# Performance work log

Measured on AMD Instinct MI355X. Metric: run time of the kernel, lower is better.

Reference implementation:

```python
import jax, jax.numpy as jnp
import numpy as np
import math

EPS = 1e-8
LN_EPS = 1e-5
B, S, E, NH = 2, 2048, 1024, 4
DH = E // NH


def setup_inputs() -> dict:
    key = jax.random.key(0)
    ks = jax.random.split(key, 7)
    std_g = math.sqrt(2.0 / (5.0 * 3 * E))
    return {
        "q": jax.random.normal(ks[0], (B, S, E), dtype=jnp.float32),
        "k": jax.random.normal(ks[1], (B, S, E), dtype=jnp.float32),
        "v": jax.random.normal(ks[2], (B, S, E), dtype=jnp.float32),
        "igate_w": jax.random.normal(ks[3], (NH, 3 * E), dtype=jnp.float32) * std_g,
        "igate_b": jax.random.normal(ks[4], (NH,), dtype=jnp.float32) * 0.1,
        "fgate_w": jax.random.normal(ks[5], (NH, 3 * E), dtype=jnp.float32) * std_g,
        "fgate_b": jnp.linspace(3.4, 6.0, NH, dtype=jnp.float32),
        "out_w": jnp.zeros((E,), dtype=jnp.float32),  # residual affine weight (scale = 1 + out_w)
    }


def _mlstm_cell(q, k, v, igate_w, igate_b, fgate_w, fgate_b, out_w):
    Bq, Sq, Eq = q.shape
    # gate pre-activations from concatenated q,k,v: [B,S,NH]
    if_in = jnp.concatenate([q, k, v], axis=-1)
    ig = jnp.einsum("bsf,hf->bsh", if_in, igate_w) + igate_b
    fg = jnp.einsum("bsf,hf->bsh", if_in, fgate_w) + fgate_b
    ig = jnp.transpose(ig, (0, 2, 1))[..., None]  # [B,NH,S,1]
    fg = jnp.transpose(fg, (0, 2, 1))[..., None]  # [B,NH,S,1]

    # split heads: [B,NH,S,DH]
    qh = q.reshape(Bq, Sq, NH, DH).transpose(0, 2, 1, 3)
    kh = k.reshape(Bq, Sq, NH, DH).transpose(0, 2, 1, 3)
    vh = v.reshape(Bq, Sq, NH, DH).transpose(0, 2, 1, 3)

    # cumulative log forget gates -> causal decay matrix (log space)
    log_fg = jax.nn.log_sigmoid(fg)                           # [B,NH,S,1]
    cs = jnp.cumsum(log_fg, axis=2)                           # [B,NH,S,1]
    cs_shift = jnp.concatenate([jnp.zeros_like(cs[:, :, :1]), cs[:, :, :-1]], axis=2)
    # log_fg_matrix[i,j] = cumsum[i] - cumsum[j-1], masked causal
    logfg_mat = cs - jnp.swapaxes(cs_shift, -2, -1)           # [B,NH,S,S]
    ltr = jnp.tril(jnp.ones((Sq, Sq), dtype=bool))
    logfg_mat = jnp.where(ltr, logfg_mat, -jnp.inf)
    log_D = logfg_mat + jnp.swapaxes(ig, -2, -1)              # + igate row broadcast [B,NH,1,S]

    max_log_D = jnp.max(log_D, axis=-1, keepdims=True)        # [B,NH,S,1]
    D = jnp.exp(log_D - max_log_D)                            # stabilized decay matrix

    qk = jnp.einsum("bhsd,bhtd->bhst", qh, kh / math.sqrt(DH))
    C = qk * D
    sum_C_abs = jnp.abs(jnp.sum(C, axis=-1, keepdims=True))
    normaliser = jnp.maximum(sum_C_abs, jnp.exp(-max_log_D))  # robust normalizer
    C_norm = C / (normaliser + EPS)
    h = jnp.einsum("bhst,bhtd->bhsd", C_norm, vh)             # [B,NH,S,DH]

    # MultiHeadLayerNorm == group_norm with NH groups, per-channel residual weight
    mean = jnp.mean(h, axis=-1, keepdims=True)
    var = jnp.mean((h - mean) ** 2, axis=-1, keepdims=True)
    h_norm = (h - mean) / jnp.sqrt(var + LN_EPS)
    scale = (1.0 + out_w).reshape(1, NH, 1, DH)
    h_norm = h_norm * scale

    return h_norm.transpose(0, 2, 1, 3).reshape(Bq, Sq, Eq)


def reference(q, k, v, igate_w, igate_b, fgate_w, fgate_b, out_w):
    return _mlstm_cell(q, k, v, igate_w, igate_b, fgate_w, fgate_b, out_w)
```

## Files before the change

kernel.cpp:

```cpp
#include <hip/hip_runtime.h>
#include <hip/hip_bf16.h>
#include <math.h>

#define Bb  2
#define Ss  2048
#define Ee  1024
#define NHh 4
#define DHh 256
#define BH  (Bb*NHh)
#define TI  64
#define TIB 128
#define TJ  32
#define NT2 (Ss/TI)
#define NTB (Ss/TIB)
#define NJT (Ss/TJ)

typedef short        s8v   __attribute__((ext_vector_type(8)));
typedef float        f4v   __attribute__((ext_vector_type(4)));
typedef float        f16v  __attribute__((ext_vector_type(16)));
typedef unsigned int u4v   __attribute__((ext_vector_type(4)));
typedef unsigned int u2v   __attribute__((ext_vector_type(2)));

__device__ inline unsigned pkbf2(float a, float b) {
    __hip_bfloat162 h2 = __float22bfloat162_rn(float2{a, b});
    unsigned u;
    __builtin_memcpy(&u, &h2, 4);
    return u;
}

__device__ inline void async16(const void* g, void* l) {
    __builtin_amdgcn_global_load_lds(
        (const __attribute__((address_space(1))) void*)g,
        (__attribute__((address_space(3))) void*)l, 16, 0, 0);
}

__global__ __launch_bounds__(256) void gates_prep_kernel(
    const float* __restrict__ q, const float* __restrict__ k, const float* __restrict__ v,
    const float* __restrict__ igw, const float* __restrict__ igb,
    const float* __restrict__ fgw, const float* __restrict__ fgb,
    float* __restrict__ ig_out, float* __restrict__ fg_out,
    unsigned short* __restrict__ Kimg, unsigned short* __restrict__ Vimg)
{
    int bidx = blockIdx.x;
    int tid = threadIdx.x;

    if (bidx >= 512) {
        int pidx = bidx - 512;
        int bh = pidx >> 6, jt = pidx & 63;
        int b = bh >> 2, h = bh & 3;
        int J0 = jt * TJ;
        const size_t hoff = (size_t)h * DHh;
        unsigned short* Kt = Kimg + (size_t)pidx * 1024 * 8;
        unsigned short* Vt = Vimg + (size_t)pidx * 1024 * 8;

        {
            int kR = tid >> 3, kc0 = tid & 7;
            const float* src = k + ((size_t)(b * Ss + J0 + kR)) * Ee + hoff;
#pragma unroll
            for (int p = 0; p < 4; p++) {
                int cc = kc0 + 8 * p;
                float4 x0 = ((const float4*)(src + cc * 8))[0];
                float4 x1 = ((const float4*)(src + cc * 8))[1];
                u4v wv;
                wv.x = pkbf2(x0.x, x0.y); wv.y = pkbf2(x0.z, x0.w);
                wv.z = pkbf2(x1.x, x1.y); wv.w = pkbf2(x1.z, x1.w);
                *(u4v*)&Kt[(kR * 32 + (cc ^ (kR & 7))) * 8] = wv;
            }
        }
        {
            int vdp = tid & 127, vjb = tid >> 7;
            int d0 = vdp * 2;
#pragma unroll
            for (int p = 0; p < 2; p++) {
                int jc = vjb + 2 * p;
                const float* vbase = v + ((size_t)(b * Ss + J0 + jc * 8)) * Ee + hoff + d0;
                float2 e0 = *(const float2*)(vbase);
                float2 e1 = *(const float2*)(vbase + Ee);
                float2 e2 = *(const float2*)(vbase + 2 * Ee);
                float2 e3 = *(const float2*)(vbase + 3 * Ee);
                float2 e4 = *(const float2*)(vbase + 4 * Ee);
                float2 e5 = *(const float2*)(vbase + 5 * Ee);
                float2 e6 = *(const float2*)(vbase + 6 * Ee);
                float2 e7 = *(const float2*)(vbase + 7 * Ee);
                int swz = jc ^ (vdp & 3);
                u4v w0, w1;
                w0.x = pkbf2(e0.x, e1.x); w0.y = pkbf2(e2.x, e3.x);
                w0.z = pkbf2(e4.x, e5.x); w0.w = pkbf2(e6.x, e7.x);
                w1.x = pkbf2(e0.y, e1.y); w1.y = pkbf2(e2.y, e3.y);
                w1.z = pkbf2(e4.y, e5.y); w1.w = pkbf2(e6.y, e7.y);
                *(u4v*)&Vt[(d0 * 4 + swz) * 8] = w0;
                *(u4v*)&Vt[((d0 + 1) * 4 + swz) * 8] = w1;
            }
        }
        return;
    }

    int sc = bidx >> 1, hp = bidx & 1;
    __shared__ float wl[4][3072];
    __shared__ float pw[4][8];

#pragma unroll
    for (int c = 0; c < 4; c++) {
        int h = hp * 2 + (c >> 1);
        const float* src = ((c & 1) ? fgw : igw) + (size_t)h * 3 * Ee;
        for (int idx = tid * 4; idx < 3 * Ee; idx += 1024)
            *(float4*)&wl[c][idx] = *(const float4*)(src + idx);
    }
    __syncthreads();

    int c4 = tid * 4;
    int w = tid >> 6, lane = tid & 63;

    for (int sp = 0; sp < 8; sp++) {
        int bs0 = sc * 16 + sp * 2;
        float4 qa = *(const float4*)(q + (size_t)bs0 * Ee + c4);
        float4 ka = *(const float4*)(k + (size_t)bs0 * Ee + c4);
        float4 va = *(const float4*)(v + (size_t)bs0 * Ee + c4);
        float4 qb = *(const float4*)(q + (size_t)(bs0 + 1) * Ee + c4);
        float4 kb = *(const float4*)(k + (size_t)(bs0 + 1) * Ee + c4);
        float4 vb = *(const float4*)(v + (size_t)(bs0 + 1) * Ee + c4);
        float red[8];
#pragma unroll
        for (int c = 0; c < 4; c++) {
            const float* wc = wl[c];
            float4 wq = *(const float4*)&wc[c4];
            float4 wk = *(const float4*)&wc[Ee + c4];
            float4 wv = *(const float4*)&wc[2 * Ee + c4];
            float x0 = qa.x*wq.x + qa.y*wq.y + qa.z*wq.z + qa.w*wq.w
                     + ka.x*wk.x + ka.y*wk.y + ka.z*wk.z + ka.w*wk.w
                     + va.x*wv.x + va.y*wv.y + va.z*wv.z + va.w*wv.w;
            float x1 = qb.x*wq.x + qb.y*wq.y + qb.z*wq.z + qb.w*wq.w
                     + kb.x*wk.x + kb.y*wk.y + kb.z*wk.z + kb.w*wk.w
                     + vb.x*wv.x + vb.y*wv.y + vb.z*wv.z + vb.w*wv.w;
            for (int off = 32; off > 0; off >>= 1) {
                x0 += __shfl_down(x0, off, 64);
                x1 += __shfl_down(x1, off, 64);
            }
            red[c] = x0; red[4 + c] = x1;
        }
        __syncthreads();
        if (lane == 0) {
#pragma unroll
            for (int c = 0; c < 8; c++) pw[w][c] = red[c];
        }
        __syncthreads();
        if (tid < 8) {
            float t = pw[0][tid] + pw[1][tid] + pw[2][tid] + pw[3][tid];
            int rr = tid >> 2, cc = tid & 3;
            int h = hp * 2 + (cc >> 1);
            int bs = bs0 + rr;
            int b = bs >> 11, s = bs & 2047;
            size_t o = ((size_t)(b * NHh + h)) * Ss + s;
            if (cc & 1) fg_out[o] = t + fgb[h];
            else        ig_out[o] = t + igb[h];
        }
    }
}

#define CHUNK 8
__global__ __launch_bounds__(256) void scan_kernel(
    const float* __restrict__ ig, const float* __restrict__ fg,
    float* __restrict__ a_out, float* __restrict__ M_out, float* __restrict__ nf_out)
{
    int bh = blockIdx.x;
    int tid = threadIdx.x;
    const float* igp = ig + (size_t)bh * Ss;
    const float* fgp = fg + (size_t)bh * Ss;
    int s0 = tid * CHUNK;

    float ls[CHUNK], cs[CHUNK];
    float tot = 0.f;
#pragma unroll
    for (int c = 0; c < CHUNK; c++) {
        float x = fgp[s0 + c];
        float l = fminf(x, 0.f) - log1pf(expf(-fabsf(x)));
        ls[c] = l; tot += l; cs[c] = tot;
    }
    __shared__ float sc[256];
    sc[tid] = tot; __syncthreads();
    for (int off = 1; off < 256; off <<= 1) {
        float add = (tid >= off) ? sc[tid - off] : 0.f;
        __syncthreads();
        sc[tid] += add;
        __syncthreads();
    }
    float excl = sc[tid] - tot;

    float av[CHUNK], pmax[CHUNK];
    float tmax = -INFINITY;
#pragma unroll
    for (int c = 0; c < CHUNK; c++) {
        float csf  = excl + cs[c];
        float csm1 = csf - ls[c];
        float a = igp[s0 + c] - csm1;
        av[c] = a;
        tmax = fmaxf(tmax, a);
        pmax[c] = tmax;
        cs[c] = csf;
    }
    __shared__ float sm[256];
    sm[tid] = tmax; __syncthreads();
    for (int off = 1; off < 256; off <<= 1) {
        float other = (tid >= off) ? sm[tid - off] : -INFINITY;
        __syncthreads();
        sm[tid] = fmaxf(sm[tid], other);
        __syncthreads();
    }
    float emax = (tid > 0) ? sm[tid - 1] : -INFINITY;
#pragma unroll
    for (int c = 0; c < CHUNK; c++) {
        float M = fmaxf(emax, pmax[c]);
        size_t o = (size_t)bh * Ss + s0 + c;
        a_out[o]  = av[c];
        M_out[o]  = M;
        nf_out[o] = expf(-cs[c] - M);
    }
}

__global__ __launch_bounds__(256, 2) void mlstm_eq(
    const float* __restrict__ qp,
    const unsigned short* __restrict__ Kimg, const unsigned short* __restrict__ Vimg,
    const float* __restrict__ a_ws, const float* __restrict__ M_ws,
    float* __restrict__ outF, float* __restrict__ Hpart, float* __restrict__ rsbuf)
{
    int bidx = blockIdx.x;
    int bh = bidx & 7;
    int w  = bidx >> 3;
    int pr = w >> 3;
    int c8 = w & 7;
    int b = bh >> 2, h = bh & 3;
    int tid = threadIdx.x;

    const int nA = 4 * pr + 4;
    const int s0 = (c8 * 68) >> 3;
    const int e0 = ((c8 + 1) * 68) >> 3;
    int qA = 0;
#pragma unroll
    for (int cc = 0; cc < 8; cc++)
        if ((((cc + 1) * 68) >> 3) <= nA) qA++;

    const size_t hoff = (size_t)h * DHh;
    const size_t HP = (size_t)Bb * Ss * Ee;

    __shared__ unsigned short KF[2][1024 * 8];
    __shared__ unsigned short VF[2][1024 * 8];
    __shared__ unsigned short PF[512 * 8];
    __shared__ float a_s[2][TJ];
    __shared__ float rs_s[TIB];

    const int iq   = tid >> 6;
    const int lane = tid & 63;
    const int lm = lane & 15, q4 = lane >> 4;
    const float inv_sqrt_dh = 0.0625f;

    const unsigned short* Kb = Kimg + (size_t)(bh * NJT) * 1024 * 8;
    const unsigned short* Vb = Vimg + (size_t)(bh * NJT) * 1024 * 8;
    const float* a_base = a_ws + (size_t)bh * Ss;

    for (int pc = 0; pc < 2; pc++) {
        int T, jt_beg, jt_end, ord;
        if (pc == 0) {
            if (s0 >= nA) continue;
            T = pr; jt_beg = s0;
            jt_end = (e0 < nA) ? e0 : nA;
            ord = c8;
        } else {
            if (e0 <= nA) continue;
            T = 15 - pr;
            jt_beg = (s0 > nA ? s0 : nA) - nA;
            jt_end = e0 - nA;
            ord = c8 - qA;
        }
        const int I0 = T * TIB;
        float* Hdst = (ord == 0) ? outF : (Hpart + (size_t)(ord - 1) * HP);

        s8v qf0[8], qf1[8];
        {
            const float* qrow0 = qp + ((size_t)(b * Ss + I0 + iq * 16 + lm)) * Ee + hoff;
            const float* qrow1 = qrow0 + (size_t)64 * Ee;
#pragma unroll
            for (int ks = 0; ks < 8; ks++) {
                const float4* p0 = (const float4*)(qrow0 + ks * 32 + q4 * 8);
                float4 x0 = p0[0], x1 = p0[1];
                union { s8v v; unsigned u[4]; } rr;
                rr.u[0] = pkbf2(x0.x, x0.y);
                rr.u[1] = pkbf2(x0.z, x0.w);
                rr.u[2] = pkbf2(x1.x, x1.y);
                rr.u[3] = pkbf2(x1.z, x1.w);
                qf0[ks] = rr.v;
                const float4* p1 = (const float4*)(qrow1 + ks * 32 + q4 * 8);
                float4 y0 = p1[0], y1 = p1[1];
                union { s8v v; unsigned u[4]; } ss;
                ss.u[0] = pkbf2(y0.x, y0.y);
                ss.u[1] = pkbf2(y0.z, y0.w);
                ss.u[2] = pkbf2(y1.x, y1.y);
                ss.u[3] = pkbf2(y1.z, y1.w);
                qf1[ks] = ss.v;
            }
        }
        const int  i_row0 = I0 + iq * 16 + lm;
        const int  i_row1 = i_row0 + 64;
        const float Mi0 = M_ws[(size_t)bh * Ss + i_row0];
        const float Mi1 = M_ws[(size_t)bh * Ss + i_row1];

        f4v acc0[16], acc1[16];
#pragma unroll
        for (int t = 0; t < 16; t++) {
            acc0[t][0]=0.f; acc0[t][1]=0.f; acc0[t][2]=0.f; acc0[t][3]=0.f;
            acc1[t][0]=0.f; acc1[t][1]=0.f; acc1[t][2]=0.f; acc1[t][3]=0.f;
        }
        float rs_a0 = 0.f, rs_a1 = 0.f;

        {
            const unsigned short* Kt = Kb + (size_t)jt_beg * 1024 * 8;
            const unsigned short* Vt = Vb + (size_t)jt_beg * 1024 * 8;
#pragma unroll
            for (int p = 0; p < 4; p++) {
                int cbase = (iq * 4 + p) * 64;
                async16(Kt + (size_t)(cbase + lane) * 8, &KF[0][cbase * 8]);
                async16(Vt + (size_t)(cbase + lane) * 8, &VF[0][cbase * 8]);
            }
            if (tid < TJ) a_s[0][tid] = a_base[jt_beg * TJ + tid];
        }

        int cur = 0;
        for (int jt = jt_beg; jt < jt_end; jt++, cur ^= 1) {
            __syncthreads();

            if (jt + 1 < jt_end) {
                const unsigned short* Kt = Kb + (size_t)(jt + 1) * 1024 * 8;
                const unsigned short* Vt = Vb + (size_t)(jt + 1) * 1024 * 8;
#pragma unroll
                for (int p = 0; p < 4; p++) {
                    int cbase = (iq * 4 + p) * 64;
                    async16(Kt + (size_t)(cbase + lane) * 8, &KF[cur ^ 1][cbase * 8]);
                    async16(Vt + (size_t)(cbase + lane) * 8, &VF[cur ^ 1][cbase * 8]);
                }
                if (tid < TJ) a_s[cur ^ 1][tid] = a_base[(jt + 1) * TJ + tid];
            }
            const int J0 = jt * TJ;

            f4v c00 = {0.f,0.f,0.f,0.f}, c01 = c00, c10 = c00, c11 = c00;
#pragma unroll
            for (int ks = 0; ks < 8; ks++) {
                int swzk = ((ks * 4 + q4) ^ (lm & 7)) * 8;
                s8v af0 = *(const s8v*)&KF[cur][(lm * 32) * 8 + swzk];
                s8v af1 = *(const s8v*)&KF[cur][((16 + lm) * 32) * 8 + swzk];
                c00 = __builtin_amdgcn_mfma_f32_16x16x32_bf16(af0, qf0[ks], c00, 0, 0, 0);
                c01 = __builtin_amdgcn_mfma_f32_16x16x32_bf16(af1, qf0[ks], c01, 0, 0, 0);
                c10 = __builtin_amdgcn_mfma_f32_16x16x32_bf16(af0, qf1[ks], c10, 0, 0, 0);
                c11 = __builtin_amdgcn_mfma_f32_16x16x32_bf16(af1, qf1[ks], c11, 0, 0, 0);
            }
            {
                float rsum0 = 0.f, rsum1 = 0.f;
#pragma unroll
                for (int t = 0; t < 2; t++) {
                    const f4v ca = t ? c01 : c00;
                    const f4v cb = t ? c11 : c10;
                    const int jb = t * 16 + q4 * 4;
                    float p0[4], p1[4];
#pragma unroll
                    for (int rr = 0; rr < 4; rr++) {
                        int jg = J0 + jb + rr;
                        float ev = __expf(a_s[cur][jb + rr] - Mi0) * inv_sqrt_dh;
                        float ev1 = __expf(a_s[cur][jb + rr] - Mi1) * inv_sqrt_dh;
                        float pv0 = 0.f, pv1 = 0.f;
                        if (jg <= i_row0) pv0 = ca[rr] * ev;
                        if (jg <= i_row1) pv1 = cb[rr] * ev1;
                        p0[rr] = pv0; rsum0 += pv0;
                        p1[rr] = pv1; rsum1 += pv1;
                    }
                    int kb = t * 2 + (q4 >> 1);
                    int cidx = (iq * 64 + lm * 4 + (kb ^ (lm & 3))) * 8 + (q4 & 1) * 4;
                    u2v pw0, pw1;
                    pw0.x = pkbf2(p0[0], p0[1]); pw0.y = pkbf2(p0[2], p0[3]);
                    pw1.x = pkbf2(p1[0], p1[1]); pw1.y = pkbf2(p1[2], p1[3]);
                    *(u2v*)&PF[cidx]            = pw0;
                    *(u2v*)&PF[256 * 8 + cidx]  = pw1;
                }
                rsum0 += __shfl_xor(rsum0, 16);
                rsum0 += __shfl_xor(rsum0, 32);
                rs_a0 += rsum0;
                rsum1 += __shfl_xor(rsum1, 16);
                rsum1 += __shfl_xor(rsum1, 32);
                rs_a1 += rsum1;
            }
            int pidx = (iq * 64 + lm * 4 + (q4 ^ (lm & 3))) * 8;
            s8v pa0 = *(const s8v*)&PF[pidx];
            s8v pa1 = *(const s8v*)&PF[256 * 8 + pidx];

#pragma unroll
            for (int db = 0; db < 16; db++) {
                int d = db * 16 + lm;
                s8v vb = *(const s8v*)&VF[cur][(d * 4 + (q4 ^ ((d >> 1) & 3))) * 8];
                acc0[db] = __builtin_amdgcn_mfma_f32_16x16x32_bf16(pa0, vb, acc0[db], 0, 0, 0);
                acc1[db] = __builtin_amdgcn_mfma_f32_16x16x32_bf16(pa1, vb, acc1[db], 0, 0, 0);
            }
        }

        if (q4 == 0) {
            rs_s[iq * 16 + lm] = rs_a0;
            rs_s[64 + iq * 16 + lm] = rs_a1;
        }
        __syncthreads();
        if (tid < TIB)
            rsbuf[(size_t)ord * BH * Ss + (size_t)bh * Ss + I0 + tid] = rs_s[tid];

#pragma unroll
        for (int rr = 0; rr < 4; rr++) {
            float* row0 = Hdst + ((size_t)(b * Ss + I0 + iq * 16 + q4 * 4 + rr)) * Ee + hoff + lm;
            float* row1 = row0 + (size_t)64 * Ee;
#pragma unroll
            for (int db = 0; db < 16; db++) {
                row0[db * 16] = acc0[db][rr];
                row1[db * 16] = acc1[db][rr];
            }
        }
    }
}

__global__ __launch_bounds__(256, 2) void mlstm_big2(
    const float* __restrict__ qp,
    const unsigned short* __restrict__ Kimg, const unsigned short* __restrict__ Vimg,
    const float* __restrict__ a_ws, const float* __restrict__ M_ws,
    float* __restrict__ outF, float* __restrict__ Hpart, float* __restrict__ rsbuf)
{
    int bidx = blockIdx.x;
    int qd = bidx >> 7, u = bidx & 127;
    int bh = u & 7;
    int r  = u >> 3;
    int T  = (qd < 2) ? (15 - r) : r;
    int sg = qd;
    int b = bh >> 2, h = bh & 3;
    int I0 = T * TIB;
    int tid = threadIdx.x;

    const int tot = 4 * T + 4;
    const int jt_beg = (sg * tot) / 4;
    const int jt_end = ((sg + 1) * tot) / 4;
    const size_t hoff = (size_t)h * DHh;
    float* Hdst = (sg == 0) ? outF : (Hpart + (size_t)(sg - 1) * Bb * Ss * Ee);

    __shared__ unsigned short KF[2][1024 * 8];
    __shared__ unsigned short VF[2][1024 * 8];
    __shared__ unsigned short PF[512 * 8];
    __shared__ float a_s[2][TJ];
    __shared__ float rs_s[TIB];

    const int iq   = tid >> 6;
    const int lane = tid & 63;
    const int lm = lane & 15, q4 = lane >> 4;

    s8v qf0[8], qf1[8];
    {
        const float* qrow0 = qp + ((size_t)(b * Ss + I0 + iq * 16 + lm)) * Ee + hoff;
        const float* qrow1 = qrow0 + (size_t)64 * Ee;
#pragma unroll
        for (int ks = 0; ks < 8; ks++) {
            const float4* p0 = (const float4*)(qrow0 + ks * 32 + q4 * 8);
            float4 x0 = p0[0], x1 = p0[1];
            union { s8v v; unsigned u[4]; } rr;
            rr.u[0] = pkbf2(x0.x, x0.y);
            rr.u[1] = pkbf2(x0.z, x0.w);
            rr.u[2] = pkbf2(x1.x, x1.y);
            rr.u[3] = pkbf2(x1.z, x1.w);
            qf0[ks] = rr.v;
            const float4* p1 = (const float4*)(qrow1 + ks * 32 + q4 * 8);
            float4 y0 = p1[0], y1 = p1[1];
            union { s8v v; unsigned u[4]; } ss;
            ss.u[0] = pkbf2(y0.x, y0.y);
            ss.u[1] = pkbf2(y0.z, y0.w);
            ss.u[2] = pkbf2(y1.x, y1.y);
            ss.u[3] = pkbf2(y1.z, y1.w);
            qf1[ks] = ss.v;
        }
    }
    const int  i_row0 = I0 + iq * 16 + lm;
    const int  i_row1 = i_row0 + 64;
    const float Mi0 = M_ws[(size_t)bh * Ss + i_row0];
    const float Mi1 = M_ws[(size_t)bh * Ss + i_row1];

    f4v acc0[16], acc1[16];
#pragma unroll
    for (int t = 0; t < 16; t++) {
        acc0[t][0]=0.f; acc0[t][1]=0.f; acc0[t][2]=0.f; acc0[t][3]=0.f;
        acc1[t][0]=0.f; acc1[t][1]=0.f; acc1[t][2]=0.f; acc1[t][3]=0.f;
    }
    float rs_a0 = 0.f, rs_a1 = 0.f;
    const float inv_sqrt_dh = 0.0625f;

    const unsigned short* Kb = Kimg + (size_t)(bh * NJT) * 1024 * 8;
    const unsigned short* Vb = Vimg + (size_t)(bh * NJT) * 1024 * 8;

    {
        const unsigned short* Kt = Kb + (size_t)jt_beg * 1024 * 8;
        const unsigned short* Vt = Vb + (size_t)jt_beg * 1024 * 8;
#pragma unroll
        for (int p = 0; p < 4; p++) {
            int cbase = (iq * 4 + p) * 64;
            async16(Kt + (size_t)(cbase + lane) * 8, &KF[0][cbase * 8]);
            async16(Vt + (size_t)(cbase + lane) * 8, &VF[0][cbase * 8]);
        }
        if (tid < TJ) a_s[0][tid] = a_ws[(size_t)bh * Ss + jt_beg * TJ + tid];
    }

    int cur = 0;
    for (int jt = jt_beg; jt < jt_end; jt++, cur ^= 1) {
        __syncthreads();

        if (jt + 1 < jt_end) {
            const unsigned short* Kt = Kb + (size_t)(jt + 1) * 1024 * 8;
            const unsigned short* Vt = Vb + (size_t)(jt + 1) * 1024 * 8;
#pragma unroll
            for (int p = 0; p < 4; p++) {
                int cbase = (iq * 4 + p) * 64;
                async16(Kt + (size_t)(cbase + lane) * 8, &KF[cur ^ 1][cbase * 8]);
                async16(Vt + (size_t)(cbase + lane) * 8, &VF[cur ^ 1][cbase * 8]);
            }
            if (tid < TJ) a_s[cur ^ 1][tid] = a_ws[(size_t)bh * Ss + (jt + 1) * TJ + tid];
        }
        const int J0 = jt * TJ;

        f4v c00 = {0.f,0.f,0.f,0.f}, c01 = c00, c10 = c00, c11 = c00;
#pragma unroll
        for (int ks = 0; ks < 8; ks++) {
            int swzk = ((ks * 4 + q4) ^ (lm & 7)) * 8;
            s8v af0 = *(const s8v*)&KF[cur][(lm * 32) * 8 + swzk];
            s8v af1 = *(const s8v*)&KF[cur][((16 + lm) * 32) * 8 + swzk];
            c00 = __builtin_amdgcn_mfma_f32_16x16x32_bf16(af0, qf0[ks], c00, 0, 0, 0);
            c01 = __builtin_amdgcn_mfma_f32_16x16x32_bf16(af1, qf0[ks], c01, 0, 0, 0);
            c10 = __builtin_amdgcn_mfma_f32_16x16x32_bf16(af0, qf1[ks], c10, 0, 0, 0);
            c11 = __builtin_amdgcn_mfma_f32_16x16x32_bf16(af1, qf1[ks], c11, 0, 0, 0);
        }
        {
            float rsum0 = 0.f, rsum1 = 0.f;
#pragma unroll
            for (int t = 0; t < 2; t++) {
                const f4v ca = t ? c01 : c00;
                const f4v cb = t ? c11 : c10;
                const int jb = t * 16 + q4 * 4;
                float p0[4], p1[4];
#pragma unroll
                for (int rr = 0; rr < 4; rr++) {
                    int jg = J0 + jb + rr;
                    float ev = __expf(a_s[cur][jb + rr] - Mi0) * inv_sqrt_dh;
                    float ev1 = __expf(a_s[cur][jb + rr] - Mi1) * inv_sqrt_dh;
                    float pv0 = 0.f, pv1 = 0.f;
                    if (jg <= i_row0) pv0 = ca[rr] * ev;
                    if (jg <= i_row1) pv1 = cb[rr] * ev1;
                    p0[rr] = pv0; rsum0 += pv0;
                    p1[rr] = pv1; rsum1 += pv1;
                }
                int kb = t * 2 + (q4 >> 1);
                int cidx = (iq * 64 + lm * 4 + (kb ^ (lm & 3))) * 8 + (q4 & 1) * 4;
                u2v pw0, pw1;
                pw0.x = pkbf2(p0[0], p0[1]); pw0.y = pkbf2(p0[2], p0[3]);
                pw1.x = pkbf2(p1[0], p1[1]); pw1.y = pkbf2(p1[2], p1[3]);
                *(u2v*)&PF[cidx]            = pw0;
                *(u2v*)&PF[256 * 8 + cidx]  = pw1;
            }
            rsum0 += __shfl_xor(rsum0, 16);
            rsum0 += __shfl_xor(rsum0, 32);
            rs_a0 += rsum0;
            rsum1 += __shfl_xor(rsum1, 16);
            rsum1 += __shfl_xor(rsum1, 32);
            rs_a1 += rsum1;
        }
        int pidx = (iq * 64 + lm * 4 + (q4 ^ (lm & 3))) * 8;
        s8v pa0 = *(const s8v*)&PF[pidx];
        s8v pa1 = *(const s8v*)&PF[256 * 8 + pidx];

#pragma unroll
        for (int db = 0; db < 16; db++) {
            int d = db * 16 + lm;
            s8v vb = *(const s8v*)&VF[cur][(d * 4 + (q4 ^ ((d >> 1) & 3))) * 8];
            acc0[db] = __builtin_amdgcn_mfma_f32_16x16x32_bf16(pa0, vb, acc0[db], 0, 0, 0);
            acc1[db] = __builtin_amdgcn_mfma_f32_16x16x32_bf16(pa1, vb, acc1[db], 0, 0, 0);
        }
    }

    if (q4 == 0) {
        rs_s[iq * 16 + lm] = rs_a0;
        rs_s[64 + iq * 16 + lm] = rs_a1;
    }
    __syncthreads();
    if (tid < TIB)
        rsbuf[(size_t)sg * BH * Ss + (size_t)bh * Ss + I0 + tid] = rs_s[tid];

#pragma unroll
    for (int rr = 0; rr < 4; rr++) {
        float* row0 = Hdst + ((size_t)(b * Ss + I0 + iq * 16 + q4 * 4 + rr)) * Ee + hoff + lm;
        float* row1 = row0 + (size_t)64 * Ee;
#pragma unroll
        for (int db = 0; db < 16; db++) {
            row0[db * 16] = acc0[db][rr];
            row1[db * 16] = acc1[db][rr];
        }
    }
}

template<int PARTS>
__global__ __launch_bounds__(256, 4) void mlstm_fallback(
    const float* __restrict__ qp, const float* __restrict__ kp, const float* __restrict__ vp,
    const float* __restrict__ a_ws, const float* __restrict__ M_ws,
    float* __restrict__ outF, float* __restrict__ Hpart, float* __restrict__ rsbuf)
{
    int bidx = blockIdx.x;
    int bh, T, sg;
    if (PARTS == 1) {
        bh = bidx & 7; T = (NT2 - 1) - (bidx >> 3); sg = 0;
    } else {
        int qd = bidx >> 8, u = bidx & 255;
        bh = u & 7;
        int r = u >> 3;
        T  = qd ? r : (31 - r);
        sg = r & 1;
    }
    int b = bh >> 2, h = bh & 3;
    int I0 = T * TI;
    int tid = threadIdx.x;

    const int tot = 2 * T + 2;
    const int jt_beg = (sg * tot) / PARTS;
    const int jt_end = ((sg + 1) * tot) / PARTS;
    const size_t hoff = (size_t)h * DHh;
    float* Hdst = (sg == 0) ? outF : (Hpart + (size_t)(sg - 1) * Bb * Ss * Ee);

    if (jt_beg >= jt_end) {
        float4 z = {0.f, 0.f, 0.f, 0.f};
        for (int t = tid; t < TI * 64; t += 256) {
            int r2 = t >> 6, c = t & 63;
            *(float4*)(Hdst + ((size_t)(b * Ss + I0 + r2)) * Ee + hoff + 4 * c) = z;
        }
        if (tid < TI) rsbuf[(size_t)sg * BH * Ss + (size_t)bh * Ss + I0 + tid] = 0.f;
        return;
    }

    __shared__ unsigned short KF[1024 * 8];
    __shared__ unsigned short VF[1024 * 8];
    __shared__ unsigned short PF[256 * 8];
    __shared__ float a_s[TJ];
    __shared__ float rs_s[TI];

    const int iq   = tid >> 6;
    const int lane = tid & 63;
    const int lm = lane & 15, q4 = lane >> 4;
    const int m5 = lane & 31, hl = lane >> 5;

    s8v qf[8];
    {
        const float* qrow = qp + ((size_t)(b * Ss + I0 + iq * 16 + lm)) * Ee + hoff;
#pragma unroll
        for (int ks = 0; ks < 8; ks++) {
            const float4* p = (const float4*)(qrow + ks * 32 + q4 * 8);
            float4 x0 = p[0], x1 = p[1];
            union { s8v v; unsigned u[4]; } rr;
            rr.u[0] = pkbf2(x0.x, x0.y);
            rr.u[1] = pkbf2(x0.z, x0.w);
            rr.u[2] = pkbf2(x1.x, x1.y);
            rr.u[3] = pkbf2(x1.z, x1.w);
            qf[ks] = rr.v;
        }
    }
    const int  i_row = I0 + iq * 16 + lm;
    const float Mi = M_ws[(size_t)bh * Ss + i_row];

    f16v acc[4];
#pragma unroll
    for (int t = 0; t < 4; t++)
#pragma unroll
        for (int i = 0; i < 16; i++) acc[t][i] = 0.f;
    float rs_acc = 0.f;

    const float inv_sqrt_dh = 0.0625f;
    const int kR  = tid >> 3, kc0 = tid & 7;
    const int vdp = tid & 127, vjb = tid >> 7;

    for (int jt = jt_beg; jt < jt_end; jt++) {
        const int J0 = jt * TJ;
        __syncthreads();
        {
            const float* src = kp + ((size_t)(b * Ss + J0 + kR)) * Ee + hoff;
#pragma unroll
            for (int p = 0; p < 4; p++) {
                int cc = kc0 + 8 * p;
                float4 x0 = ((const float4*)(src + cc * 8))[0];
                float4 x1 = ((const float4*)(src + cc * 8))[1];
                u4v wv;
                wv.x = pkbf2(x0.x, x0.y); wv.y = pkbf2(x0.z, x0.w);
                wv.z = pkbf2(x1.x, x1.y); wv.w = pkbf2(x1.z, x1.w);
                *(u4v*)&KF[(kR * 32 + (cc ^ (kR & 7))) * 8] = wv;
            }
            int d0 = vdp * 2;
#pragma unroll
            for (int p = 0; p < 2; p++) {
                int jc = vjb + 2 * p;
                const float* vbase = vp + ((size_t)(b * Ss + J0 + jc * 8)) * Ee + hoff + d0;
                float2 e0 = *(const float2*)(vbase);
                float2 e1 = *(const float2*)(vbase + Ee);
                float2 e2 = *(const float2*)(vbase + 2 * Ee);
                float2 e3 = *(const float2*)(vbase + 3 * Ee);
                float2 e4 = *(const float2*)(vbase + 4 * Ee);
                float2 e5 = *(const float2*)(vbase + 5 * Ee);
                float2 e6 = *(const float2*)(vbase + 6 * Ee);
                float2 e7 = *(const float2*)(vbase + 7 * Ee);
                int swz = jc ^ (vdp & 3);
                u4v w0, w1;
                w0.x = pkbf2(e0.x, e1.x); w0.y = pkbf2(e2.x, e3.x);
                w0.z = pkbf2(e4.x, e5.x); w0.w = pkbf2(e6.x, e7.x);
                w1.x = pkbf2(e0.y, e1.y); w1.y = pkbf2(e2.y, e3.y);
                w1.z = pkbf2(e4.y, e5.y); w1.w = pkbf2(e6.y, e7.y);
                *(u4v*)&VF[(d0 * 4 + swz) * 8] = w0;
                *(u4v*)&VF[((d0 + 1) * 4 + swz) * 8] = w1;
            }
        }
        if (tid < TJ) a_s[tid] = a_ws[(size_t)bh * Ss + J0 + tid];
        __syncthreads();

        f4v c0 = {0.f, 0.f, 0.f, 0.f}, c1 = c0;
#pragma unroll
        for (int ks = 0; ks < 8; ks++) {
            int swzk = ((ks * 4 + q4) ^ (lm & 7)) * 8;
            s8v af0 = *(const s8v*)&KF[(lm * 32) * 8 + swzk];
            s8v af1 = *(const s8v*)&KF[((16 + lm) * 32) * 8 + swzk];
            c0 = __builtin_amdgcn_mfma_f32_16x16x32_bf16(af0, qf[ks], c0, 0, 0, 0);
            c1 = __builtin_amdgcn_mfma_f32_16x16x32_bf16(af1, qf[ks], c1, 0, 0, 0);
        }
        {
            float rsum = 0.f;
#pragma unroll
            for (int t = 0; t < 2; t++) {
                const f4v cc = t ? c1 : c0;
                const int jb = t * 16 + q4 * 4;
                float p[4];
#pragma unroll
                for (int rr = 0; rr < 4; rr++) {
                    int jg = J0 + jb + rr;
                    float pv = 0.f;
                    if (jg <= i_row) pv = cc[rr] * inv_sqrt_dh * __expf(a_s[jb + rr] - Mi);
                    p[rr] = pv; rsum += pv;
                }
                u2v pwv;
                pwv.x = pkbf2(p[0], p[1]);
                pwv.y = pkbf2(p[2], p[3]);
                int i = iq * 16 + lm;
                int kb = t * 2 + (q4 >> 1);
                *(u2v*)&PF[(i * 4 + (kb ^ ((i >> 1) & 3))) * 8 + (q4 & 1) * 4] = pwv;
            }
            rsum += __shfl_xor(rsum, 16);
            rsum += __shfl_xor(rsum, 32);
            rs_acc += rsum;
        }
        __syncthreads();

#pragma unroll
        for (int ks2 = 0; ks2 < 2; ks2++) {
            int swz2 = ((ks2 * 2 + hl) ^ ((m5 >> 1) & 3)) * 8;
            s8v pa0 = *(const s8v*)&PF[(m5 * 4) * 8 + swz2];
            s8v pa1 = *(const s8v*)&PF[((32 + m5) * 4) * 8 + swz2];
            s8v vb0 = *(const s8v*)&VF[((iq * 32 + m5) * 4) * 8 + swz2];
            s8v vb1 = *(const s8v*)&VF[(((iq + 4) * 32 + m5) * 4) * 8 + swz2];
            acc[0] = __builtin_amdgcn_mfma_f32_32x32x16_bf16(pa0, vb0, acc[0], 0, 0, 0);
            acc[1] = __builtin_amdgcn_mfma_f32_32x32x16_bf16(pa0, vb1, acc[1], 0, 0, 0);
            acc[2] = __builtin_amdgcn_mfma_f32_32x32x16_bf16(pa1, vb0, acc[2], 0, 0, 0);
            acc[3] = __builtin_amdgcn_mfma_f32_32x32x16_bf16(pa1, vb1, acc[3], 0, 0, 0);
        }
    }

    if (q4 == 0) rs_s[iq * 16 + lm] = rs_acc;
    __syncthreads();
    if (tid < TI)
        rsbuf[(size_t)sg * BH * Ss + (size_t)bh * Ss + I0 + tid] = rs_s[tid];

#pragma unroll
    for (int im = 0; im < 2; im++)
#pragma unroll
        for (int ns = 0; ns < 2; ns++) {
            const f16v av = acc[im * 2 + ns];
            const int col = (iq + 4 * ns) * 32 + m5;
#pragma unroll
            for (int rr = 0; rr < 16; rr++) {
                int row = I0 + im * 32 + (rr & 3) + 8 * (rr >> 2) + 4 * hl;
                Hdst[((size_t)(b * Ss + row)) * Ee + hoff + col] = av[rr];
            }
        }
}

__global__ __launch_bounds__(256) void combine_var(
    const float* __restrict__ Hb, const float* __restrict__ rsbuf,
    const float* __restrict__ nf_ws, const float* __restrict__ out_w,
    float* __restrict__ outF)
{
    int rid = blockIdx.x * 4 + (threadIdx.x >> 6);
    int lane = threadIdx.x & 63;
    int bh = rid >> 11, s = rid & 2047;
    int b = bh >> 2, h = bh & 3;
    int T = s >> 7;
    int p;
    if (T <= 7) {
        int nA = 4 * T + 4;
        p = 0;
#pragma unroll
        for (int cc = 0; cc < 8; cc++)
            if (((cc * 68) >> 3) < nA) p++;
    } else {
        int nA = 64 - 4 * T;
        int q = 0;
#pragma unroll
        for (int cc = 0; cc < 8; cc++)
            if ((((cc + 1) * 68) >> 3) <= nA) q++;
        p = 8 - q;
    }

    size_t base = ((size_t)(b * Ss + s)) * Ee + (size_t)h * DHh + lane * 4;
    const size_t HP = (size_t)Bb * Ss * Ee;
    float4 ha = *(const float4*)(outF + base);
    float rs = rsbuf[(size_t)bh * Ss + s];
    for (int k = 1; k < p; k++) {
        float4 hb = *(const float4*)(Hb + (size_t)(k - 1) * HP + base);
        ha.x += hb.x; ha.y += hb.y; ha.z += hb.z; ha.w += hb.w;
        rs += rsbuf[(size_t)k * BH * Ss + (size_t)bh * Ss + s];
    }
    float nfv = nf_ws[(size_t)bh * Ss + s];
    float invn = 1.f / (fmaxf(fabsf(rs), nfv) + 1e-8f);
    float4 x;
    x.x = ha.x * invn; x.y = ha.y * invn; x.z = ha.z * invn; x.w = ha.w * invn;
    float sx = x.x + x.y + x.z + x.w;
    float sq = x.x*x.x + x.y*x.y + x.z*x.z + x.w*x.w;
#pragma unroll
    for (int off = 1; off < 64; off <<= 1) {
        sx += __shfl_xor(sx, off);
        sq += __shfl_xor(sq, off);
    }
    float mean = sx * (1.f / DHh);
    float var  = sq * (1.f / DHh) - mean * mean;
    float rstd = rsqrtf(var + 1e-5f);
    float4 w4 = *(const float4*)(out_w + (size_t)h * DHh + lane * 4);
    float4 o;
    o.x = (x.x - mean) * rstd * (1.f + w4.x);
    o.y = (x.y - mean) * rstd * (1.f + w4.y);
    o.z = (x.z - mean) * rstd * (1.f + w4.z);
    o.w = (x.w - mean) * rstd * (1.f + w4.w);
    *(float4*)(outF + base) = o;
}

template<int PARTS>
__global__ __launch_bounds__(256) void combine_kernel(
    const float* __restrict__ Hb, const float* __restrict__ rsbuf,
    const float* __restrict__ nf_ws, const float* __restrict__ out_w,
    float* __restrict__ outF)
{
    int rid = blockIdx.x * 4 + (threadIdx.x >> 6);
    int lane = threadIdx.x & 63;
    int bh = rid >> 11, s = rid & 2047;
    int b = bh >> 2, h = bh & 3;
    size_t base = ((size_t)(b * Ss + s)) * Ee + (size_t)h * DHh + lane * 4;
    float4 ha = *(const float4*)(outF + base);
    float rs = rsbuf[(size_t)bh * Ss + s];
#pragma unroll
    for (int k = 1; k < PARTS; k++) {
        float4 hb = *(const float4*)(Hb + (size_t)(k - 1) * Bb * Ss * Ee + base);
        ha.x += hb.x; ha.y += hb.y; ha.z += hb.z; ha.w += hb.w;
        rs += rsbuf[(size_t)k * BH * Ss + (size_t)bh * Ss + s];
    }
    float nfv = nf_ws[(size_t)bh * Ss + s];
    float invn = 1.f / (fmaxf(fabsf(rs), nfv) + 1e-8f);
    float4 x;
    x.x = ha.x * invn; x.y = ha.y * invn; x.z = ha.z * invn; x.w = ha.w * invn;
    float sx = x.x + x.y + x.z + x.w;
    float sq = x.x*x.x + x.y*x.y + x.z*x.z + x.w*x.w;
#pragma unroll
    for (int off = 1; off < 64; off <<= 1) {
        sx += __shfl_xor(sx, off);
        sq += __shfl_xor(sq, off);
    }
    float mean = sx * (1.f / DHh);
    float var  = sq * (1.f / DHh) - mean * mean;
    float rstd = rsqrtf(var + 1e-5f);
    float4 w4 = *(const float4*)(out_w + (size_t)h * DHh + lane * 4);
    float4 o;
    o.x = (x.x - mean) * rstd * (1.f + w4.x);
    o.y = (x.y - mean) * rstd * (1.f + w4.y);
    o.z = (x.z - mean) * rstd * (1.f + w4.z);
    o.w = (x.w - mean) * rstd * (1.f + w4.w);
    *(float4*)(outF + base) = o;
}

extern "C" void kernel_launch(void* const* d_in, const int* in_sizes, int n_in,
                              void* d_out, int out_size, void* d_ws, size_t ws_size,
                              hipStream_t stream) {
    const float* q   = (const float*)d_in[0];
    const float* k   = (const float*)d_in[1];
    const float* v   = (const float*)d_in[2];
    const float* igw = (const float*)d_in[3];
    const float* igb = (const float*)d_in[4];
    const float* fgw = (const float*)d_in[5];
    const float* fgb = (const float*)d_in[6];
    const float* ow  = (const float*)d_in[7];
    float* out = (float*)d_out;

    float* ws = (float*)d_ws;
    float* ig = ws;
    float* fg = ws + 16384;
    float* aa = ws + 32768;
    float* MM = ws + 49152;
    float* nf = ws + 65536;
    float* rsb = ws + 81920;
    const size_t base_f = 81920 + 131072;
    unsigned short* KimgP = (unsigned short*)(ws + base_f);
    const size_t img_u = (size_t)BH * NJT * 1024 * 8;
    unsigned short* VimgP = KimgP + img_u;
    float* HpartImg = (float*)(VimgP + img_u);
    float* HpartRaw = ws + base_f;
    const size_t HP = (size_t)Bb * Ss * Ee;

    const size_t need_eq = base_f * 4 + 2 * img_u * 2 + 7 * HP * 4;
    const size_t need4   = base_f * 4 + 2 * img_u * 2 + 3 * HP * 4;
    const size_t need2   = base_f * 4 + 1 * HP * 4;

    if (ws_size >= need_eq) {
        gates_prep_kernel<<<1024, 256, 0, stream>>>(q, k, v, igw, igb, fgw, fgb,
                                                    ig, fg, KimgP, VimgP);
        scan_kernel<<<BH, 256, 0, stream>>>(ig, fg, aa, MM, nf);
        mlstm_eq<<<512, 256, 0, stream>>>(q, KimgP, VimgP, aa, MM,
                                          out, HpartImg, rsb);
        combine_var<<<BH * Ss / 4, 256, 0, stream>>>(HpartImg, rsb, nf, ow, out);
    } else if (ws_size >= need4) {
        gates_prep_kernel<<<1024, 256, 0, stream>>>(q, k, v, igw, igb, fgw, fgb,
                                                    ig, fg, KimgP, VimgP);
        scan_kernel<<<BH, 256, 0, stream>>>(ig, fg, aa, MM, nf);
        mlstm_big2<<<512, 256, 0, stream>>>(q, KimgP, VimgP, aa, MM,
                                            out, HpartImg, rsb);
        combine_kernel<4><<<BH * Ss / 4, 256, 0, stream>>>(HpartImg, rsb, nf, ow, out);
    } else if (ws_size >= need2) {
        gates_prep_kernel<<<512, 256, 0, stream>>>(q, k, v, igw, igb, fgw, fgb,
                                                   ig, fg, nullptr, nullptr);
        scan_kernel<<<BH, 256, 0, stream>>>(ig, fg, aa, MM, nf);
        mlstm_fallback<2><<<512, 256, 0, stream>>>(q, k, v, aa, MM, out, HpartRaw, rsb);
        combine_kernel<2><<<BH * Ss / 4, 256, 0, stream>>>(HpartRaw, rsb, nf, ow, out);
    } else {
        gates_prep_kernel<<<512, 256, 0, stream>>>(q, k, v, igw, igb, fgw, fgb,
                                                   ig, fg, nullptr, nullptr);
        scan_kernel<<<BH, 256, 0, stream>>>(ig, fg, aa, MM, nf);
        mlstm_fallback<1><<<256, 256, 0, stream>>>(q, k, v, aa, MM, out, HpartRaw, rsb);
        combine_kernel<1><<<BH * Ss / 4, 256, 0, stream>>>(HpartRaw, rsb, nf, ow, out);
    }
}
```

Measured before the change: 218.2 us.

## Rebalance mLSTM attention into equal 11-tile chunks with 64-row query tiles

Replaces the paired 128-row tile scheme with 64-row query tiles whose causal key-tile work (2T+2 tiles per row tile) is flattened and split into 96 equal chunks of 11 tiles per head. That gives 768 blocks, and launch bounds rise to 3 blocks per CU because of smaller register and LDS footprints. The change also drops the K/V double buffering in favour of issuing the V load during QK compute, and adds s_setprio around the MFMA loops. The combine kernel computes the partial count from the new chunk mapping. This trades per-block reuse and double-buffered prefetch for finer load balance and higher occupancy, with up to 6 partial buffers.

```diff
diff --git a/kernel.cpp b/kernel.cpp
--- a/kernel.cpp
+++ b/kernel.cpp
@@ -12,7 +12,6 @@
 #define TIB 128
 #define TJ  32
 #define NT2 (Ss/TI)
-#define NTB (Ss/TIB)
 #define NJT (Ss/TJ)
 
 typedef short        s8v   __attribute__((ext_vector_type(8)));
@@ -217,7 +216,7 @@
     }
 }
 
-__global__ __launch_bounds__(256, 2) void mlstm_eq(
+__global__ __launch_bounds__(256, 3) void mlstm_ch(
     const float* __restrict__ qp,
     const unsigned short* __restrict__ Kimg, const unsigned short* __restrict__ Vimg,
     const float* __restrict__ a_ws, const float* __restrict__ M_ws,
@@ -225,28 +224,18 @@
 {
     int bidx = blockIdx.x;
     int bh = bidx & 7;
-    int w  = bidx >> 3;
-    int pr = w >> 3;
-    int c8 = w & 7;
+    int c  = bidx >> 3;
     int b = bh >> 2, h = bh & 3;
     int tid = threadIdx.x;
 
-    const int nA = 4 * pr + 4;
-    const int s0 = (c8 * 68) >> 3;
-    const int e0 = ((c8 + 1) * 68) >> 3;
-    int qA = 0;
-#pragma unroll
-    for (int cc = 0; cc < 8; cc++)
-        if ((((cc + 1) * 68) >> 3) <= nA) qA++;
-
     const size_t hoff = (size_t)h * DHh;
     const size_t HP = (size_t)Bb * Ss * Ee;
 
-    __shared__ unsigned short KF[2][1024 * 8];
-    __shared__ unsigned short VF[2][1024 * 8];
-    __shared__ unsigned short PF[512 * 8];
-    __shared__ float a_s[2][TJ];
-    __shared__ float rs_s[TIB];
+    __shared__ unsigned short KF[1024 * 8];
+    __shared__ unsigned short VF[1024 * 8];
+    __shared__ unsigned short PF[256 * 8];
+    __shared__ float a_s[TJ];
+    __shared__ float rs_s[TI];
 
     const int iq   = tid >> 6;
     const int lane = tid & 63;
@@ -257,165 +246,145 @@
     const unsigned short* Vb = Vimg + (size_t)(bh * NJT) * 1024 * 8;
     const float* a_base = a_ws + (size_t)bh * Ss;
 
-    for (int pc = 0; pc < 2; pc++) {
-        int T, jt_beg, jt_end, ord;
-        if (pc == 0) {
-            if (s0 >= nA) continue;
-            T = pr; jt_beg = s0;
-            jt_end = (e0 < nA) ? e0 : nA;
-            ord = c8;
-        } else {
-            if (e0 <= nA) continue;
-            T = 15 - pr;
-            jt_beg = (s0 > nA ? s0 : nA) - nA;
-            jt_end = e0 - nA;
-            ord = c8 - qA;
-        }
-        const int I0 = T * TIB;
+    int g    = c * 11;
+    int gend = g + 11;
+    int T = (int)((sqrtf((float)(4 * g + 1)) - 1.f) * 0.5f);
+    while (T * (T + 1) > g) T--;
+    while ((T + 1) * (T + 2) <= g) T++;
+
+    while (g < gend) {
+        const int tstart = T * (T + 1);
+        const int tend   = tstart + 2 * T + 2;
+        const int jt_beg = g - tstart;
+        const int pend   = (gend < tend) ? gend : tend;
+        const int jt_end = pend - tstart;
+        const int ord    = c - tstart / 11;
+        const int I0     = T * TI;
         float* Hdst = (ord == 0) ? outF : (Hpart + (size_t)(ord - 1) * HP);
 
-        s8v qf0[8], qf1[8];
+        s8v qf[8];
         {
-            const float* qrow0 = qp + ((size_t)(b * Ss + I0 + iq * 16 + lm)) * Ee + hoff;
-            const float* qrow1 = qrow0 + (size_t)64 * Ee;
+            const float* qrow = qp + ((size_t)(b * Ss + I0 + iq * 16 + lm)) * Ee + hoff;
 #pragma unroll
             for (int ks = 0; ks < 8; ks++) {
-                const float4* p0 = (const float4*)(qrow0 + ks * 32 + q4 * 8);
-                float4 x0 = p0[0], x1 = p0[1];
+                const float4* p = (const float4*)(qrow + ks * 32 + q4 * 8);
+                float4 x0 = p[0], x1 = p[1];
                 union { s8v v; unsigned u[4]; } rr;
                 rr.u[0] = pkbf2(x0.x, x0.y);
                 rr.u[1] = pkbf2(x0.z, x0.w);
                 rr.u[2] = pkbf2(x1.x, x1.y);
                 rr.u[3] = pkbf2(x1.z, x1.w);
-                qf0[ks] = rr.v;
-                const float4* p1 = (const float4*)(qrow1 + ks * 32 + q4 * 8);
-                float4 y0 = p1[0], y1 = p1[1];
-                union { s8v v; unsigned u[4]; } ss;
-                ss.u[0] = pkbf2(y0.x, y0.y);
-                ss.u[1] = pkbf2(y0.z, y0.w);
-                ss.u[2] = pkbf2(y1.x, y1.y);
-                ss.u[3] = pkbf2(y1.z, y1.w);
-                qf1[ks] = ss.v;
-            }
-        }
-        const int  i_row0 = I0 + iq * 16 + lm;
-        const int  i_row1 = i_row0 + 64;
-        const float Mi0 = M_ws[(size_t)bh * Ss + i_row0];
-        const float Mi1 = M_ws[(size_t)bh * Ss + i_row1];
-
-        f4v acc0[16], acc1[16];
-#pragma unroll
-        for (int t = 0; t < 16; t++) {
-            acc0[t][0]=0.f; acc0[t][1]=0.f; acc0[t][2]=0.f; acc0[t][3]=0.f;
-            acc1[t][0]=0.f; acc1[t][1]=0.f; acc1[t][2]=0.f; acc1[t][3]=0.f;
-        }
-        float rs_a0 = 0.f, rs_a1 = 0.f;
+                qf[ks] = rr.v;
+            }
+        }
+        const int  i_row = I0 + iq * 16 + lm;
+        const float Mi = M_ws[(size_t)bh * Ss + i_row];
+
+        f4v acc[16];
+#pragma unroll
+        for (int t = 0; t < 16; t++) { acc[t][0]=0.f; acc[t][1]=0.f; acc[t][2]=0.f; acc[t][3]=0.f; }
+        float rs_acc = 0.f;
 
         {
             const unsigned short* Kt = Kb + (size_t)jt_beg * 1024 * 8;
-            const unsigned short* Vt = Vb + (size_t)jt_beg * 1024 * 8;
 #pragma unroll
             for (int p = 0; p < 4; p++) {
                 int cbase = (iq * 4 + p) * 64;
-                async16(Kt + (size_t)(cbase + lane) * 8, &KF[0][cbase * 8]);
-                async16(Vt + (size_t)(cbase + lane) * 8, &VF[0][cbase * 8]);
-            }
-            if (tid < TJ) a_s[0][tid] = a_base[jt_beg * TJ + tid];
-        }
-
-        int cur = 0;
-        for (int jt = jt_beg; jt < jt_end; jt++, cur ^= 1) {
+                async16(Kt + (size_t)(cbase + lane) * 8, &KF[cbase * 8]);
+            }
+            if (lane < 2)
+                async16(a_base + (size_t)jt_beg * TJ + iq * 8 + lane * 4, &a_s[iq * 8]);
+        }
+        __syncthreads();
+
+        for (int jt = jt_beg; jt < jt_end; jt++) {
+            {
+                const unsigned short* Vt = Vb + (size_t)jt * 1024 * 8;
+#pragma unroll
+                for (int p = 0; p < 4; p++) {
+                    int cbase = (iq * 4 + p) * 64;
+                    async16(Vt + (size_t)(cbase + lane) * 8, &VF[cbase * 8]);
+                }
+            }
+            const int J0 = jt * TJ;
+
+            f4v c0 = {0.f, 0.f, 0.f, 0.f}, c1 = c0;
+            __builtin_amdgcn_s_setprio(1);
+#pragma unroll
+            for (int ks = 0; ks < 8; ks++) {
+                int swzk = ((ks * 4 + q4) ^ (lm & 7)) * 8;
+                s8v af0 = *(const s8v*)&KF[(lm * 32) * 8 + swzk];
+                s8v af1 = *(const s8v*)&KF[((16 + lm) * 32) * 8 + swzk];
+                c0 = __builtin_amdgcn_mfma_f32_16x16x32_bf16(af0, qf[ks], c0, 0, 0, 0);
+                c1 = __builtin_amdgcn_mfma_f32_16x16x32_bf16(af1, qf[ks], c1, 0, 0, 0);
+            }
+            __builtin_amdgcn_s_setprio(0);
+            {
+                float rsum = 0.f;
+#pragma unroll
+                for (int t = 0; t < 2; t++) {
+                    const f4v cc = t ? c1 : c0;
+                    const int jb = t * 16 + q4 * 4;
+                    float p[4];
+#pragma unroll
+                    for (int rr = 0; rr < 4; rr++) {
+                        int jg = J0 + jb + rr;
+                        float pv = 0.f;
+                        if (jg <= i_row) pv = cc[rr] * inv_sqrt_dh * __expf(a_s[jb + rr] - Mi);
+                        p[rr] = pv; rsum += pv;
+                    }
+                    u2v pwv;
+                    pwv.x = pkbf2(p[0], p[1]);
+                    pwv.y = pkbf2(p[2], p[3]);
+                    int kb = t * 2 + (q4 >> 1);
+                    *(u2v*)&PF[(iq * 64 + lm * 4 + (kb ^ (lm & 3))) * 8 + (q4 & 1) * 4] = pwv;
+                }
+                rsum += __shfl_xor(rsum, 16);
+                rsum += __shfl_xor(rsum, 32);
+                rs_acc += rsum;
+            }
+            s8v pa = *(const s8v*)&PF[(iq * 64 + lm * 4 + (q4 ^ (lm & 3))) * 8];
+
             __syncthreads();
 
             if (jt + 1 < jt_end) {
                 const unsigned short* Kt = Kb + (size_t)(jt + 1) * 1024 * 8;
-                const unsigned short* Vt = Vb + (size_t)(jt + 1) * 1024 * 8;
 #pragma unroll
                 for (int p = 0; p < 4; p++) {
                     int cbase = (iq * 4 + p) * 64;
-                    async16(Kt + (size_t)(cbase + lane) * 8, &KF[cur ^ 1][cbase * 8]);
-                    async16(Vt + (size_t)(cbase + lane) * 8, &VF[cur ^ 1][cbase * 8]);
+                    async16(Kt + (size_t)(cbase + lane) * 8, &KF[cbase * 8]);
                 }
-                if (tid < TJ) a_s[cur ^ 1][tid] = a_base[(jt + 1) * TJ + tid];
-            }
-            const int J0 = jt * TJ;
-
-            f4v c00 = {0.f,0.f,0.f,0.f}, c01 = c00, c10 = c00, c11 = c00;
-#pragma unroll
-            for (int ks = 0; ks < 8; ks++) {
-                int swzk = ((ks * 4 + q4) ^ (lm & 7)) * 8;
-                s8v af0 = *(const s8v*)&KF[cur][(lm * 32) * 8 + swzk];
-                s8v af1 = *(const s8v*)&KF[cur][((16 + lm) * 32) * 8 + swzk];
-                c00 = __builtin_amdgcn_mfma_f32_16x16x32_bf16(af0, qf0[ks], c00, 0, 0, 0);
-                c01 = __builtin_amdgcn_mfma_f32_16x16x32_bf16(af1, qf0[ks], c01, 0, 0, 0);
-                c10 = __builtin_amdgcn_mfma_f32_16x16x32_bf16(af0, qf1[ks], c10, 0, 0, 0);
-                c11 = __builtin_amdgcn_mfma_f32_16x16x32_bf16(af1, qf1[ks], c11, 0, 0, 0);
-            }
-            {
-                float rsum0 = 0.f, rsum1 = 0.f;
-#pragma unroll
-                for (int t = 0; t < 2; t++) {
-                    const f4v ca = t ? c01 : c00;
-                    const f4v cb = t ? c11 : c10;
-                    const int jb = t * 16 + q4 * 4;
-                    float p0[4], p1[4];
-#pragma unroll
-                    for (int rr = 0; rr < 4; rr++) {
-                        int jg = J0 + jb + rr;
-                        float ev = __expf(a_s[cur][jb + rr] - Mi0) * inv_sqrt_dh;
-                        float ev1 = __expf(a_s[cur][jb + rr] - Mi1) * inv_sqrt_dh;
-                        float pv0 = 0.f, pv1 = 0.f;
-                        if (jg <= i_row0) pv0 = ca[rr] * ev;
-                        if (jg <= i_row1) pv1 = cb[rr] * ev1;
-                        p0[rr] = pv0; rsum0 += pv0;
-                        p1[rr] = pv1; rsum1 += pv1;
-                    }
-                    int kb = t * 2 + (q4 >> 1);
-                    int cidx = (iq * 64 + lm * 4 + (kb ^ (lm & 3))) * 8 + (q4 & 1) * 4;
-                    u2v pw0, pw1;
-                    pw0.x = pkbf2(p0[0], p0[1]); pw0.y = pkbf2(p0[2], p0[3]);
-                    pw1.x = pkbf2(p1[0], p1[1]); pw1.y = pkbf2(p1[2], p1[3]);
-                    *(u2v*)&PF[cidx]            = pw0;
-                    *(u2v*)&PF[256 * 8 + cidx]  = pw1;
-                }
-                rsum0 += __shfl_xor(rsum0, 16);
-                rsum0 += __shfl_xor(rsum0, 32);
-                rs_a0 += rsum0;
-                rsum1 += __shfl_xor(rsum1, 16);
-                rsum1 += __shfl_xor(rsum1, 32);
-                rs_a1 += rsum1;
-            }
-            int pidx = (iq * 64 + lm * 4 + (q4 ^ (lm & 3))) * 8;
-            s8v pa0 = *(const s8v*)&PF[pidx];
-            s8v pa1 = *(const s8v*)&PF[256 * 8 + pidx];
-
+                if (lane < 2)
+                    async16(a_base + (size_t)(jt + 1) * TJ + iq * 8 + lane * 4, &a_s[iq * 8]);
+            }
+
+            __builtin_amdgcn_s_setprio(1);
 #pragma unroll
             for (int db = 0; db < 16; db++) {
                 int d = db * 16 + lm;
-                s8v vb = *(const s8v*)&VF[cur][(d * 4 + (q4 ^ ((d >> 1) & 3))) * 8];
-                acc0[db] = __builtin_amdgcn_mfma_f32_16x16x32_bf16(pa0, vb, acc0[db], 0, 0, 0);
-                acc1[db] = __builtin_amdgcn_mfma_f32_16x16x32_bf16(pa1, vb, acc1[db], 0, 0, 0);
-            }
-        }
-
-        if (q4 == 0) {
-            rs_s[iq * 16 + lm] = rs_a0;
-            rs_s[64 + iq * 16 + lm] = rs_a1;
-        }
-        __syncthreads();
-        if (tid < TIB)
+                s8v vb = *(const s8v*)&VF[(d * 4 + (q4 ^ ((d >> 1) & 3))) * 8];
+                acc[db] = __builtin_amdgcn_mfma_f32_16x16x32_bf16(pa, vb, acc[db], 0, 0, 0);
+            }
+            __builtin_amdgcn_s_setprio(0);
+
+            __syncthreads();
+        }
+
+        if (q4 == 0) rs_s[iq * 16 + lm] = rs_acc;
+        __syncthreads();
+        if (tid < TI)
             rsbuf[(size_t)ord * BH * Ss + (size_t)bh * Ss + I0 + tid] = rs_s[tid];
 
 #pragma unroll
         for (int rr = 0; rr < 4; rr++) {
-            float* row0 = Hdst + ((size_t)(b * Ss + I0 + iq * 16 + q4 * 4 + rr)) * Ee + hoff + lm;
-            float* row1 = row0 + (size_t)64 * Ee;
-#pragma unroll
-            for (int db = 0; db < 16; db++) {
-                row0[db * 16] = acc0[db][rr];
-                row1[db * 16] = acc1[db][rr];
-            }
-        }
+            float* row = Hdst + ((size_t)(b * Ss + I0 + iq * 16 + q4 * 4 + rr)) * Ee + hoff + lm;
+#pragma unroll
+            for (int db = 0; db < 16; db++)
+                row[db * 16] = acc[db][rr];
+        }
+
+        g = pend;
+        if (g >= tend) T++;
     }
 }
 
@@ -786,7 +755,7 @@
         }
 }
 
-__global__ __launch_bounds__(256) void combine_var(
+__global__ __launch_bounds__(256) void combine_ch(
     const float* __restrict__ Hb, const float* __restrict__ rsbuf,
     const float* __restrict__ nf_ws, const float* __restrict__ out_w,
     float* __restrict__ outF)
@@ -795,22 +764,10 @@
     int lane = threadIdx.x & 63;
     int bh = rid >> 11, s = rid & 2047;
     int b = bh >> 2, h = bh & 3;
-    int T = s >> 7;
-    int p;
-    if (T <= 7) {
-        int nA = 4 * T + 4;
-        p = 0;
-#pragma unroll
-        for (int cc = 0; cc < 8; cc++)
-            if (((cc * 68) >> 3) < nA) p++;
-    } else {
-        int nA = 64 - 4 * T;
-        int q = 0;
-#pragma unroll
-        for (int cc = 0; cc < 8; cc++)
-            if ((((cc + 1) * 68) >> 3) <= nA) q++;
-        p = 8 - q;
-    }
+    int T = s >> 6;
+    int tstart = T * (T + 1);
+    int tend   = tstart + 2 * T + 2;
+    int p = (tend - 1) / 11 - tstart / 11 + 1;
 
     size_t base = ((size_t)(b * Ss + s)) * Ee + (size_t)h * DHh + lane * 4;
     const size_t HP = (size_t)Bb * Ss * Ee;
@@ -914,17 +871,17 @@
     float* HpartRaw = ws + base_f;
     const size_t HP = (size_t)Bb * Ss * Ee;
 
-    const size_t need_eq = base_f * 4 + 2 * img_u * 2 + 7 * HP * 4;
+    const size_t need_ch = base_f * 4 + 2 * img_u * 2 + 6 * HP * 4;
     const size_t need4   = base_f * 4 + 2 * img_u * 2 + 3 * HP * 4;
     const size_t need2   = base_f * 4 + 1 * HP * 4;
 
-    if (ws_size >= need_eq) {
+    if (ws_size >= need_ch) {
         gates_prep_kernel<<<1024, 256, 0, stream>>>(q, k, v, igw, igb, fgw, fgb,
                                                     ig, fg, KimgP, VimgP);
         scan_kernel<<<BH, 256, 0, stream>>>(ig, fg, aa, MM, nf);
-        mlstm_eq<<<512, 256, 0, stream>>>(q, KimgP, VimgP, aa, MM,
+        mlstm_ch<<<768, 256, 0, stream>>>(q, KimgP, VimgP, aa, MM,
                                           out, HpartImg, rsb);
-        combine_var<<<BH * Ss / 4, 256, 0, stream>>>(HpartImg, rsb, nf, ow, out);
+        combine_ch<<<BH * Ss / 4, 256, 0, stream>>>(HpartImg, rsb, nf, ow, out);
     } else if (ws_size >= need4) {
         gates_prep_kernel<<<1024, 256, 0, stream>>>(q, k, v, igw, igb, fgw, fgb,
                                                     ig, fg, KimgP, VimgP);
```

Measured after the change: 186.7 us. -14.4%, faster.
